# Performance work log

Hardware: AMD Instinct MI355X
Metric: run time of the kernel (lower is better)

## Reference

```python
import jax, jax.numpy as jnp
import numpy as np

E = 512    # len_embeddings
T = 32     # tokennum
H = 256    # hidden_unit
IT = 5     # ICI iterations
B = 4096   # batch
EPS = 1e-6


def setup_inputs() -> dict:
    key = jax.random.key(0)
    k0, k1, k2, k3, k4 = jax.random.split(key, 5)
    x = jax.random.normal(k0, (B, E), dtype=jnp.float32)
    glorot = np.sqrt(2.0 / (E + H)).astype(np.float32)
    w_in = jax.random.normal(k1, (T, E, H), dtype=jnp.float32) * glorot
    w_val = jax.random.normal(k2, (T, E, H), dtype=jnp.float32) * glorot
    # alphas: per-token, per-iteration inhibition strengths (trained; sample nonzero)
    alphas = jax.random.uniform(k3, (T, IT), dtype=jnp.float32) * 0.5
    # scales: per-token output scale (init 1.0, perturb slightly)
    scales = 1.0 + 0.1 * jax.random.normal(k4, (T, H), dtype=jnp.float32)
    gamma = jnp.ones((T, H), dtype=jnp.float32)
    beta = jnp.zeros((T, H), dtype=jnp.float32)
    return {"x": x, "w_in": w_in, "w_val": w_val, "alphas": alphas,
            "scales": scales, "gamma": gamma, "beta": beta}


def reference(x, w_in, w_val, alphas, scales, gamma, beta):
    # batched per-token projection: [B,E] x [T,E,H] -> [B,T,H]
    hidden = jnp.einsum('be,teh->bth', x, w_in)
    # iterative competitive inhibition (fixed small IT loop)
    x_t = jax.nn.relu(hidden)
    for i in range(alphas.shape[1]):
        m = jnp.mean(x_t, axis=-1, keepdims=True)          # [B,T,1]
        a = alphas[:, i][None, :, None]                     # [1,T,1]
        x_t = jax.nn.relu(x_t - a * m)
    sparse_g = scales[None] * x_t                           # [B,T,H]
    # gated value path
    value = jnp.einsum('be,teh->bth', x, w_val)
    s = sparse_g * value
    # per-token LayerNorm over hidden dim, eps=1e-6
    mu = jnp.mean(s, axis=-1, keepdims=True)
    var = jnp.mean((s - mu) ** 2, axis=-1, keepdims=True)
    out = (s - mu) / jnp.sqrt(var + EPS) * gamma[None] + beta[None]
    return out  # [B, T, H]
```

## Files before the change

### kernel.cpp

```cpp
#include <hip/hip_runtime.h>
#include <cstdint>

using u16 = unsigned short;
using u32 = unsigned int;

constexpr int kB  = 4096;
constexpr int kE  = 512;
constexpr int kT  = 32;
constexpr int kH  = 256;
constexpr int kIT = 5;
constexpr float kEPS = 1e-6f;

typedef __attribute__((ext_vector_type(8)))  short short8;
typedef __attribute__((ext_vector_type(16))) float floatx16;
typedef __attribute__((ext_vector_type(8)))  u16   ushort8;
typedef __attribute__((ext_vector_type(4)))  float floatv4;

__device__ __forceinline__ u16 f2bf(float f) {
  u32 u = __builtin_bit_cast(u32, f);
  return (u16)((u + 0x7fffu + ((u >> 16) & 1u)) >> 16);
}

__device__ __forceinline__ floatx16 mfma32(short8 a, short8 b, floatx16 c) {
  return __builtin_amdgcn_mfma_f32_32x32x16_bf16(a, b, c, 0, 0, 0);
}

__device__ __forceinline__ void ntstore4(float* p, float4 v) {
  __builtin_nontemporal_store(__builtin_bit_cast(floatv4, v), (floatv4*)p);
}

__device__ __forceinline__ void gload16(const u16* gsrc, u16* ldst) {
  __builtin_amdgcn_global_load_lds(
      (const __attribute__((address_space(1))) u32*)gsrc,
      (__attribute__((address_space(3))) u32*)ldst, 16, 0, 0);
}

__global__ __launch_bounds__(256) void pack_x_kernel(
    const float* __restrict__ x, u16* __restrict__ xp) {
  __shared__ __attribute__((aligned(16))) float tile[64 * 132];
  const int slab = blockIdx.x >> 2;
  const int kg   = blockIdx.x & 3;
  const int tid  = threadIdx.x;

  const int r0 = tid >> 5;
  const int c0 = (tid & 31) * 4;
#pragma unroll
  for (int p = 0; p < 8; ++p) {
    const int r = p * 8 + r0;
    const float4 v = *(const float4*)(x + (size_t)(slab * 64 + r) * kE + kg * 128 + c0);
    *(float4*)(tile + r * 132 + c0) = v;
  }
  __syncthreads();

  const int wv = tid >> 6, lane = tid & 63;
#pragma unroll
  for (int q = 0; q < 4; ++q) {
    const int cc   = wv * 4 + q;
    const int ks_l = cc >> 1;
    const int mt   = cc & 1;
    const int rl   = mt * 32 + (lane & 31);
    const int kl   = ks_l * 16 + (lane >> 5) * 8;
    const float4 f0 = *(const float4*)(tile + rl * 132 + kl);
    const float4 f1 = *(const float4*)(tile + rl * 132 + kl + 4);
    ushort8 o;
    o[0] = f2bf(f0.x); o[1] = f2bf(f0.y); o[2] = f2bf(f0.z); o[3] = f2bf(f0.w);
    o[4] = f2bf(f1.x); o[5] = f2bf(f1.y); o[6] = f2bf(f1.z); o[7] = f2bf(f1.w);
    const int c = slab * 64 + (kg * 8 + ks_l) * 2 + mt;
    *(ushort8*)(xp + (size_t)c * 512 + lane * 8) = o;
  }
}

__global__ __launch_bounds__(256) void pack_w_kernel(
    const float* __restrict__ w_in, const float* __restrict__ w_val,
    u16* __restrict__ wp) {
  __shared__ __attribute__((aligned(16))) float tile[64 * 68];
  const int wb   = blockIdx.x;
  const int tl   = wb & 31;
  const int et   = tl >> 2;
  const int ht   = tl & 3;
  const int tm   = wb >> 5;
  const int t    = tm >> 1, mat = tm & 1;
  const int tid  = threadIdx.x;
  const float* src = (mat ? w_val : w_in) + (size_t)t * kE * kH +
                     (size_t)(et * 64) * kH + ht * 64;
  const int lrow = tid >> 4, lc4 = (tid & 15) * 4;
#pragma unroll
  for (int p = 0; p < 4; ++p) {
    const int e = lrow + p * 16;
    const float4 v = *(const float4*)(src + (size_t)e * kH + lc4);
    tile[e * 68 + lc4 + 0] = v.x; tile[e * 68 + lc4 + 1] = v.y;
    tile[e * 68 + lc4 + 2] = v.z; tile[e * 68 + lc4 + 3] = v.w;
  }
  __syncthreads();
  const int ks_l = tid >> 6, lane = tid & 63;
  const int kloc = ks_l * 16 + (lane >> 5) * 8;
#pragma unroll
  for (int nt_l = 0; nt_l < 2; ++nt_l) {
    const int nloc = nt_l * 32 + (lane & 31);
    ushort8 o;
#pragma unroll
    for (int j = 0; j < 8; ++j) o[j] = f2bf(tile[(kloc + j) * 68 + nloc]);
    const int c = t * 512 + (et * 4 + ks_l) * 16 + (ht * 2 + nt_l) * 2 + mat;
    *(ushort8*)(wp + (size_t)c * 512 + lane * 8) = o;
  }
}

__global__ __launch_bounds__(512, 4) void fused_kernel(
    const u16* __restrict__ xp, const u16* __restrict__ wp,
    const float* __restrict__ alphas, const float* __restrict__ scales,
    const float* __restrict__ gamma, const float* __restrict__ beta,
    float* __restrict__ out) {
  __shared__ __attribute__((aligned(16))) u16 sB[2][16 * 512];
  float* sAcc = (float*)sB;

  const int tid  = threadIdx.x;
  const int wv   = tid >> 6;
  const int lane = tid & 63;
  const int l31  = lane & 31;
  const int h    = lane >> 5;
  const int wm   = wv >> 2;
  const int wn   = wv & 3;

  const int bid  = blockIdx.x;
  const int xcd  = bid & 7;
  const int r_   = bid >> 3;
  const int st   = r_ >> 6;
  const int wi   = r_ & 63;
  const int t    = xcd * 4 + (wi >> 4);
  const int slab = st * 16 + (wi & 15);

  const u16* xsrc = xp + (size_t)slab * (32 * 2 * 512) + lane * 8;
  const u16* wsrc = wp + (size_t)t * (32 * 16 * 512) + lane * 8;

  floatx16 ai[2], av[2];
#pragma unroll
  for (int n = 0; n < 2; ++n) { ai[n] = (floatx16)0.f; av[n] = (floatx16)0.f; }

  short8 A[2];

  auto stageB = [&](int p, int buf) {
    const int cb = wv * 2;
    gload16(wsrc + (size_t)(p * 16 + cb) * 512,     &sB[buf][cb * 512]);
    gload16(wsrc + (size_t)(p * 16 + cb + 1) * 512, &sB[buf][(cb + 1) * 512]);
  };

  stageB(0, 0);
  A[0] = *(const short8*)(xsrc + 0 * 1024 + wm * 512);

#pragma unroll
  for (int p = 0; p < 32; ++p) {
    if (p < 31) {
      stageB(p + 1, (p + 1) & 1);
      A[(p + 1) & 1] = *(const short8*)(xsrc + (size_t)(p + 1) * 1024 + wm * 512);
    }
    if (p < 31) { asm volatile("s_waitcnt vmcnt(3)" ::: "memory"); }
    else        { asm volatile("s_waitcnt vmcnt(0)" ::: "memory"); }
    __builtin_amdgcn_sched_barrier(0);
    __builtin_amdgcn_s_barrier();
    __builtin_amdgcn_sched_barrier(0);

    const u16* sBp = &sB[p & 1][0] + lane * 8;
    const short8 BI0 = *(const short8*)(sBp + ((wn * 2 + 0) * 2 + 0) * 512);
    const short8 BV0 = *(const short8*)(sBp + ((wn * 2 + 0) * 2 + 1) * 512);
    const short8 BI1 = *(const short8*)(sBp + ((wn * 2 + 1) * 2 + 0) * 512);
    const short8 BV1 = *(const short8*)(sBp + ((wn * 2 + 1) * 2 + 1) * 512);
    const short8 Ac = A[p & 1];
    ai[0] = mfma32(Ac, BI0, ai[0]);
    av[0] = mfma32(Ac, BV0, av[0]);
    ai[1] = mfma32(Ac, BI1, ai[1]);
    av[1] = mfma32(Ac, BV1, av[1]);
    __builtin_amdgcn_sched_barrier(0);
    __builtin_amdgcn_s_barrier();
  }

  const float inv_h = 1.0f / kH;
  float al[kIT];
#pragma unroll
  for (int i = 0; i < kIT; ++i) al[i] = alphas[t * kIT + i] * inv_h;

  const int row_r = tid >> 4;
  const int seg   = tid & 15;
  const int r4    = (row_r & 7) << 2;

#pragma unroll
  for (int mt = 0; mt < 2; ++mt) {
    __syncthreads();
    if (wm == mt) {
#pragma unroll
      for (int nt = 0; nt < 2; ++nt)
#pragma unroll
        for (int q = 0; q < 16; ++q) {
          const int r   = (q & 3) + 8 * (q >> 2) + 4 * h;
          const int col = wn * 64 + nt * 32 + l31;
          sAcc[r * 256 + (col ^ ((r & 7) << 2))] = ai[nt][q];
        }
    }
    __syncthreads();

    float4 xt[4];
#pragma unroll
    for (int j = 0; j < 4; ++j) {
      xt[j] = *(const float4*)(sAcc + row_r * 256 + ((seg * 16 + 4 * j) ^ r4));
#pragma unroll
      for (int i = 0; i < 4; ++i) xt[j][i] = fmaxf(xt[j][i], 0.f);
    }

#pragma unroll
    for (int it = 0; it < kIT; ++it) {
      float4 s4 = xt[0];
#pragma unroll
      for (int j = 1; j < 4; ++j) s4 += xt[j];
      float v = s4.x + s4.y + s4.z + s4.w;
      v += __shfl_xor(v, 1, 16);
      v += __shfl_xor(v, 2, 16);
      v += __shfl_xor(v, 4, 16);
      v += __shfl_xor(v, 8, 16);
      const float m = al[it] * v;
#pragma unroll
      for (int j = 0; j < 4; ++j)
#pragma unroll
        for (int i = 0; i < 4; ++i) xt[j][i] = fmaxf(xt[j][i] - m, 0.f);
    }

    __syncthreads();
    if (wm == mt) {
#pragma unroll
      for (int nt = 0; nt < 2; ++nt)
#pragma unroll
        for (int q = 0; q < 16; ++q) {
          const int r   = (q & 3) + 8 * (q >> 2) + 4 * h;
          const int col = wn * 64 + nt * 32 + l31;
          sAcc[r * 256 + (col ^ ((r & 7) << 2))] = av[nt][q];
        }
    }
    __syncthreads();

    float4 res[4];
    float sum = 0.f, ssq = 0.f;
#pragma unroll
    for (int j = 0; j < 4; ++j) {
      const int lc = seg * 16 + 4 * j;
      const int cb = lc ^ r4;
      const float4 a4 = *(const float4*)(sAcc + row_r * 256 + cb);
      const float4 sc = *(const float4*)(scales + t * kH + lc);
      float4 s;
#pragma unroll
      for (int i = 0; i < 4; ++i) {
        s[i] = sc[i] * xt[j][i] * a4[i];
        sum += s[i];
        ssq += s[i] * s[i];
      }
      res[j] = s;
    }
    sum += __shfl_xor(sum, 1, 16);  ssq += __shfl_xor(ssq, 1, 16);
    sum += __shfl_xor(sum, 2, 16);  ssq += __shfl_xor(ssq, 2, 16);
    sum += __shfl_xor(sum, 4, 16);  ssq += __shfl_xor(ssq, 4, 16);
    sum += __shfl_xor(sum, 8, 16);  ssq += __shfl_xor(ssq, 8, 16);
    const float mu  = sum * inv_h;
    const float var = ssq * inv_h - mu * mu;
    const float rs  = rsqrtf(var + kEPS);

#pragma unroll
    for (int j = 0; j < 4; ++j) {
      const int lc = seg * 16 + 4 * j;
      const int cb = lc ^ r4;
      const float4 g4 = *(const float4*)(gamma + t * kH + lc);
      const float4 b4 = *(const float4*)(beta + t * kH + lc);
      float4 o;
#pragma unroll
      for (int i = 0; i < 4; ++i) o[i] = (res[j][i] - mu) * rs * g4[i] + b4[i];
      *(float4*)(sAcc + row_r * 256 + cb) = o;
    }
    __syncthreads();

#pragma unroll
    for (int r8 = 0; r8 < 4; ++r8) {
      const int rr = wv * 4 + r8;
      const int rb = (rr & 7) << 2;
      const float4 v = *(const float4*)(sAcc + rr * 256 + ((4 * lane) ^ rb));
      ntstore4(out + (size_t)(slab * 64 + mt * 32 + rr) * (kT * kH) + t * kH + 4 * lane, v);
    }
  }
}

extern "C" void kernel_launch(void* const* d_in, const int* in_sizes, int n_in,
                              void* d_out, int out_size, void* d_ws, size_t ws_size,
                              hipStream_t stream) {
  const float* x      = (const float*)d_in[0];
  const float* w_in   = (const float*)d_in[1];
  const float* w_val  = (const float*)d_in[2];
  const float* alphas = (const float*)d_in[3];
  const float* scales = (const float*)d_in[4];
  const float* gamma  = (const float*)d_in[5];
  const float* beta   = (const float*)d_in[6];
  float* out = (float*)d_out;

  u16* xp = (u16*)d_ws;
  u16* wp = xp + (size_t)64 * 32 * 2 * 512;

  pack_x_kernel<<<256, 256, 0, stream>>>(x, xp);
  pack_w_kernel<<<2048, 256, 0, stream>>>(w_in, w_val, wp);
  fused_kernel<<<kT * (kB / 64), 512, 0, stream>>>(xp, wp, alphas, scales,
                                                   gamma, beta, out);
}
```

Baseline: 343.0 us.

## Enlarge fused tile to 128 rows with 1024 threads and LDS-staged A operand

Each block now covers 128 batch rows instead of 64 and runs 1024 threads (16 waves), so every weight tile staged in LDS is reused by twice as many rows. The A operand (packed x) is also staged through LDS instead of being loaded per wave from global memory, and each stage covers two k-slices, halving the number of barrier-separated pipeline steps. Global load roles are split across waves (3 or 2 slots each) with per-wave vmcnt waits. The cost is a larger LDS footprint per block and a halved grid, which can lower occupancy and raise per-barrier synchronisation cost.

```diff
diff --git a/kernel.cpp b/kernel.cpp
--- a/kernel.cpp
+++ b/kernel.cpp
@@ -105,70 +105,86 @@
   }
 }
 
-__global__ __launch_bounds__(512, 4) void fused_kernel(
+__global__ __launch_bounds__(1024, 4) void fused_kernel(
     const u16* __restrict__ xp, const u16* __restrict__ wp,
     const float* __restrict__ alphas, const float* __restrict__ scales,
     const float* __restrict__ gamma, const float* __restrict__ beta,
     float* __restrict__ out) {
-  __shared__ __attribute__((aligned(16))) u16 sB[2][16 * 512];
-  float* sAcc = (float*)sB;
+  __shared__ __attribute__((aligned(16))) u16 sStage[2][40 * 512];
+  float* sAcc = (float*)sStage;
 
   const int tid  = threadIdx.x;
   const int wv   = tid >> 6;
   const int lane = tid & 63;
   const int l31  = lane & 31;
   const int h    = lane >> 5;
-  const int wm   = wv >> 2;
+  const int wm4  = wv >> 2;
   const int wn   = wv & 3;
 
   const int bid  = blockIdx.x;
   const int xcd  = bid & 7;
   const int r_   = bid >> 3;
-  const int st   = r_ >> 6;
-  const int wi   = r_ & 63;
-  const int t    = xcd * 4 + (wi >> 4);
-  const int slab = st * 16 + (wi & 15);
-
-  const u16* xsrc = xp + (size_t)slab * (32 * 2 * 512) + lane * 8;
-  const u16* wsrc = wp + (size_t)t * (32 * 16 * 512) + lane * 8;
+  const int st   = r_ >> 5;
+  const int wi   = r_ & 31;
+  const int t    = xcd * 4 + (wi >> 3);
+  const int sl2  = st * 8 + (wi & 7);
+
+  const int nrole = (wv < 8) ? 3 : 2;
+  const int s0    = (wv < 8) ? (wv * 3) : (24 + (wv - 8) * 2);
+  const u16* rsrc[3]; int rstride[3]; int rslot[3];
+#pragma unroll
+  for (int r = 0; r < 3; ++r) {
+    int s = s0 + r; if (s > 39) s = 39;
+    rslot[r] = s;
+    if (s < 8) {
+      const int ksl = s >> 2, m4 = s & 3;
+      rsrc[r] = xp + (size_t)((sl2 * 2 + (m4 >> 1)) * 64 + ksl * 2 + (m4 & 1)) * 512
+                   + lane * 8;
+      rstride[r] = 4 * 512;
+    } else {
+      const int b = s - 8;
+      rsrc[r] = wp + (size_t)t * (512 * 512) + (size_t)b * 512 + lane * 8;
+      rstride[r] = 32 * 512;
+    }
+  }
 
   floatx16 ai[2], av[2];
 #pragma unroll
   for (int n = 0; n < 2; ++n) { ai[n] = (floatx16)0.f; av[n] = (floatx16)0.f; }
 
-  short8 A[2];
-
-  auto stageB = [&](int p, int buf) {
-    const int cb = wv * 2;
-    gload16(wsrc + (size_t)(p * 16 + cb) * 512,     &sB[buf][cb * 512]);
-    gload16(wsrc + (size_t)(p * 16 + cb + 1) * 512, &sB[buf][(cb + 1) * 512]);
+  auto stage = [&](int P, int buf) {
+    u16* dbase = &sStage[buf][0];
+#pragma unroll
+    for (int r = 0; r < 3; ++r)
+      if (r < nrole)
+        gload16(rsrc[r] + (size_t)P * rstride[r], dbase + rslot[r] * 512);
   };
 
-  stageB(0, 0);
-  A[0] = *(const short8*)(xsrc + 0 * 1024 + wm * 512);
-
-#pragma unroll
-  for (int p = 0; p < 32; ++p) {
-    if (p < 31) {
-      stageB(p + 1, (p + 1) & 1);
-      A[(p + 1) & 1] = *(const short8*)(xsrc + (size_t)(p + 1) * 1024 + wm * 512);
-    }
-    if (p < 31) { asm volatile("s_waitcnt vmcnt(3)" ::: "memory"); }
-    else        { asm volatile("s_waitcnt vmcnt(0)" ::: "memory"); }
+  stage(0, 0);
+
+#pragma unroll
+  for (int P = 0; P < 16; ++P) {
+    if (P < 15) stage(P + 1, (P + 1) & 1);
+    if (P < 15) {
+      if (wv < 8) { asm volatile("s_waitcnt vmcnt(3)" ::: "memory"); }
+      else        { asm volatile("s_waitcnt vmcnt(2)" ::: "memory"); }
+    } else        { asm volatile("s_waitcnt vmcnt(0)" ::: "memory"); }
     __builtin_amdgcn_sched_barrier(0);
     __builtin_amdgcn_s_barrier();
     __builtin_amdgcn_sched_barrier(0);
 
-    const u16* sBp = &sB[p & 1][0] + lane * 8;
-    const short8 BI0 = *(const short8*)(sBp + ((wn * 2 + 0) * 2 + 0) * 512);
-    const short8 BV0 = *(const short8*)(sBp + ((wn * 2 + 0) * 2 + 1) * 512);
-    const short8 BI1 = *(const short8*)(sBp + ((wn * 2 + 1) * 2 + 0) * 512);
-    const short8 BV1 = *(const short8*)(sBp + ((wn * 2 + 1) * 2 + 1) * 512);
-    const short8 Ac = A[p & 1];
-    ai[0] = mfma32(Ac, BI0, ai[0]);
-    av[0] = mfma32(Ac, BV0, av[0]);
-    ai[1] = mfma32(Ac, BI1, ai[1]);
-    av[1] = mfma32(Ac, BV1, av[1]);
+    const u16* bb = &sStage[P & 1][0] + lane * 8;
+#pragma unroll
+    for (int ksl = 0; ksl < 2; ++ksl) {
+      const short8 Ac = *(const short8*)(bb + (ksl * 4 + wm4) * 512);
+#pragma unroll
+      for (int nt = 0; nt < 2; ++nt) {
+        const short8 BIc = *(const short8*)(bb + (8 + ksl * 16 + (wn * 2 + nt) * 2 + 0) * 512);
+        const short8 BVc = *(const short8*)(bb + (8 + ksl * 16 + (wn * 2 + nt) * 2 + 1) * 512);
+        ai[nt] = mfma32(Ac, BIc, ai[nt]);
+        av[nt] = mfma32(Ac, BVc, av[nt]);
+      }
+    }
     __builtin_amdgcn_sched_barrier(0);
     __builtin_amdgcn_s_barrier();
   }
@@ -178,14 +194,14 @@
 #pragma unroll
   for (int i = 0; i < kIT; ++i) al[i] = alphas[t * kIT + i] * inv_h;
 
-  const int row_r = tid >> 4;
-  const int seg   = tid & 15;
+  const int row_r = tid >> 5;
+  const int seg   = tid & 31;
   const int r4    = (row_r & 7) << 2;
 
 #pragma unroll
-  for (int mt = 0; mt < 2; ++mt) {
-    __syncthreads();
-    if (wm == mt) {
+  for (int mt4 = 0; mt4 < 4; ++mt4) {
+    __syncthreads();
+    if (wm4 == mt4) {
 #pragma unroll
       for (int nt = 0; nt < 2; ++nt)
 #pragma unroll
@@ -197,33 +213,32 @@
     }
     __syncthreads();
 
-    float4 xt[4];
-#pragma unroll
-    for (int j = 0; j < 4; ++j) {
-      xt[j] = *(const float4*)(sAcc + row_r * 256 + ((seg * 16 + 4 * j) ^ r4));
+    float4 xt[2];
+#pragma unroll
+    for (int j = 0; j < 2; ++j) {
+      xt[j] = *(const float4*)(sAcc + row_r * 256 + ((seg * 8 + 4 * j) ^ r4));
 #pragma unroll
       for (int i = 0; i < 4; ++i) xt[j][i] = fmaxf(xt[j][i], 0.f);
     }
 
 #pragma unroll
     for (int it = 0; it < kIT; ++it) {
-      float4 s4 = xt[0];
-#pragma unroll
-      for (int j = 1; j < 4; ++j) s4 += xt[j];
+      float4 s4 = xt[0] + xt[1];
       float v = s4.x + s4.y + s4.z + s4.w;
-      v += __shfl_xor(v, 1, 16);
-      v += __shfl_xor(v, 2, 16);
-      v += __shfl_xor(v, 4, 16);
-      v += __shfl_xor(v, 8, 16);
+      v += __shfl_xor(v, 1, 32);
+      v += __shfl_xor(v, 2, 32);
+      v += __shfl_xor(v, 4, 32);
+      v += __shfl_xor(v, 8, 32);
+      v += __shfl_xor(v, 16, 32);
       const float m = al[it] * v;
 #pragma unroll
-      for (int j = 0; j < 4; ++j)
+      for (int j = 0; j < 2; ++j)
 #pragma unroll
         for (int i = 0; i < 4; ++i) xt[j][i] = fmaxf(xt[j][i] - m, 0.f);
     }
 
     __syncthreads();
-    if (wm == mt) {
+    if (wm4 == mt4) {
 #pragma unroll
       for (int nt = 0; nt < 2; ++nt)
 #pragma unroll
@@ -235,11 +250,11 @@
     }
     __syncthreads();
 
-    float4 res[4];
+    float4 res[2];
     float sum = 0.f, ssq = 0.f;
 #pragma unroll
-    for (int j = 0; j < 4; ++j) {
-      const int lc = seg * 16 + 4 * j;
+    for (int j = 0; j < 2; ++j) {
+      const int lc = seg * 8 + 4 * j;
       const int cb = lc ^ r4;
       const float4 a4 = *(const float4*)(sAcc + row_r * 256 + cb);
       const float4 sc = *(const float4*)(scales + t * kH + lc);
@@ -252,17 +267,18 @@
       }
       res[j] = s;
     }
-    sum += __shfl_xor(sum, 1, 16);  ssq += __shfl_xor(ssq, 1, 16);
-    sum += __shfl_xor(sum, 2, 16);  ssq += __shfl_xor(ssq, 2, 16);
-    sum += __shfl_xor(sum, 4, 16);  ssq += __shfl_xor(ssq, 4, 16);
-    sum += __shfl_xor(sum, 8, 16);  ssq += __shfl_xor(ssq, 8, 16);
+    sum += __shfl_xor(sum, 1, 32);   ssq += __shfl_xor(ssq, 1, 32);
+    sum += __shfl_xor(sum, 2, 32);   ssq += __shfl_xor(ssq, 2, 32);
+    sum += __shfl_xor(sum, 4, 32);   ssq += __shfl_xor(ssq, 4, 32);
+    sum += __shfl_xor(sum, 8, 32);   ssq += __shfl_xor(ssq, 8, 32);
+    sum += __shfl_xor(sum, 16, 32);  ssq += __shfl_xor(ssq, 16, 32);
     const float mu  = sum * inv_h;
     const float var = ssq * inv_h - mu * mu;
     const float rs  = rsqrtf(var + kEPS);
 
 #pragma unroll
-    for (int j = 0; j < 4; ++j) {
-      const int lc = seg * 16 + 4 * j;
+    for (int j = 0; j < 2; ++j) {
+      const int lc = seg * 8 + 4 * j;
       const int cb = lc ^ r4;
       const float4 g4 = *(const float4*)(gamma + t * kH + lc);
       const float4 b4 = *(const float4*)(beta + t * kH + lc);
@@ -274,11 +290,11 @@
     __syncthreads();
 
 #pragma unroll
-    for (int r8 = 0; r8 < 4; ++r8) {
-      const int rr = wv * 4 + r8;
+    for (int k = 0; k < 2; ++k) {
+      const int rr = (tid >> 6) + k * 16;
       const int rb = (rr & 7) << 2;
       const float4 v = *(const float4*)(sAcc + rr * 256 + ((4 * lane) ^ rb));
-      ntstore4(out + (size_t)(slab * 64 + mt * 32 + rr) * (kT * kH) + t * kH + 4 * lane, v);
+      ntstore4(out + (size_t)(sl2 * 128 + mt4 * 32 + rr) * (kT * kH) + t * kH + 4 * lane, v);
     }
   }
 }
@@ -300,6 +316,6 @@
 
   pack_x_kernel<<<256, 256, 0, stream>>>(x, xp);
   pack_w_kernel<<<2048, 256, 0, stream>>>(w_in, w_val, wp);
-  fused_kernel<<<kT * (kB / 64), 512, 0, stream>>>(xp, wp, alphas, scales,
-                                                   gamma, beta, out);
-}
+  fused_kernel<<<kT * (kB / 128), 1024, 0, stream>>>(xp, wp, alphas, scales,
+                                                     gamma, beta, out);
+}
```

Result: faster. 329.5 us (-3.9%).
